# Optimization experiments

Hardware: AMD Instinct MI355X
Metric: run time of the kernel (lower is better)

Reference implementation:

```python
import jax, jax.numpy as jnp
import numpy as np

B, S, D, H, E, K = 4, 4096, 256, 1024, 8, 2


def setup_inputs() -> dict:
    key = jax.random.key(0)
    ks = jax.random.split(key, 7)
    sc = 0.02
    return {
        "x": jax.random.normal(ks[0], (B, S, D), dtype=jnp.float32),
        "w_router": jax.random.normal(ks[1], (D, E), dtype=jnp.float32) * sc,
        "b_router": jnp.zeros((E,), dtype=jnp.float32),
        "w1": jax.random.normal(ks[2], (E, D, H), dtype=jnp.float32) * sc,
        "b1": jnp.zeros((E, H), dtype=jnp.float32),
        "w2": jax.random.normal(ks[3], (E, H, D), dtype=jnp.float32) * sc,
        "b2": jnp.zeros((E, D), dtype=jnp.float32),
    }


def reference(x, w_router, b_router, w1, b1, w2, b2):
    # Router: softmax over experts, then top-k selection + renormalization
    router_logits = jnp.einsum("bsd,de->bse", x, w_router) + b_router
    router_probs = jax.nn.softmax(router_logits, axis=-1)            # [B,S,E]
    top_probs, top_idx = jax.lax.top_k(router_probs, K)               # [B,S,K]
    top_w = top_probs / jnp.sum(top_probs, axis=-1, keepdims=True)    # renorm

    # Combine weights per expert: sum_k one_hot(idx_k) * w_k  -> [B,S,E]
    combine = jnp.sum(jax.nn.one_hot(top_idx, E, dtype=x.dtype) * top_w[..., None], axis=-2)

    # Dense equivalent of the masked gather/scatter dispatch:
    # out[b,s] = sum_e combine[b,s,e] * Expert_e(x[b,s])
    h = jax.nn.gelu(jnp.einsum("bsd,edh->bseh", x, w1) + b1, approximate=False)  # [B,S,E,H]
    y = jnp.einsum("bseh,ehd->bsed", h, w2) + b2                                  # [B,S,E,D]
    out = jnp.einsum("bsed,bse->bsd", y, combine)                                  # [B,S,D]
    return out, router_probs
```

## Files before the change

### kernel.cpp

```cpp
#include <hip/hip_runtime.h>

typedef float f32x4 __attribute__((ext_vector_type(4)));
typedef short s16x8 __attribute__((ext_vector_type(8)));

static constexpr int NTOK = 16384;
static constexpr int D    = 256;
static constexpr int H    = 1024;
static constexpr int E    = 8;

__device__ __forceinline__ float bf2f(unsigned short u) {
    return __uint_as_float(((unsigned int)u) << 16);
}
__device__ __forceinline__ unsigned short f2bf(float f) {
    unsigned int u = __float_as_uint(f);
    u += 0x7FFFu + ((u >> 16) & 1u);
    return (unsigned short)(u >> 16);
}
__device__ __forceinline__ s16x8 pack8(float4 a, float4 b) {
    s16x8 v;
    v[0] = (short)f2bf(a.x); v[1] = (short)f2bf(a.y);
    v[2] = (short)f2bf(a.z); v[3] = (short)f2bf(a.w);
    v[4] = (short)f2bf(b.x); v[5] = (short)f2bf(b.y);
    v[6] = (short)f2bf(b.z); v[7] = (short)f2bf(b.w);
    return v;
}

__device__ __forceinline__ void barrier_lds_only() {
    __asm__ __volatile__("s_waitcnt lgkmcnt(0)" ::: "memory");
    __builtin_amdgcn_s_barrier();
    __asm__ __volatile__("" ::: "memory");
}

__global__ void __launch_bounds__(256) prep_kernel(
    const float* __restrict__ w1, const float* __restrict__ w2,
    unsigned short* __restrict__ w1t, unsigned short* __restrict__ w2t,
    const float* __restrict__ x, const float* __restrict__ wr,
    const float* __restrict__ br, float* __restrict__ probs_out,
    int* __restrict__ cnt, int* __restrict__ list, float* __restrict__ wlist)
{
    __shared__ __align__(16) char smem[9280];
    const int tid = threadIdx.x;

    if (blockIdx.x < 4096) {
        unsigned short (*tile)[33] = reinterpret_cast<unsigned short(*)[33]>(smem);
        int b = blockIdx.x;
        const float* src; unsigned short* dst;
        int Rr, Cc, tr, tc;
        if (b < 2048) {
            int e = b >> 8, tt = b & 255;
            Rr = 256; Cc = 1024; tr = tt >> 5; tc = tt & 31;
            src = w1 + (size_t)e * Rr * Cc; dst = w1t + (size_t)e * Rr * Cc;
        } else {
            b -= 2048;
            int e = b >> 8, tt = b & 255;
            Rr = 1024; Cc = 256; tr = tt >> 3; tc = tt & 7;
            src = w2 + (size_t)e * Rr * Cc; dst = w2t + (size_t)e * Rr * Cc;
        }
        const int c = tid & 31, r0 = tid >> 5;
        #pragma unroll
        for (int rr = 0; rr < 32; rr += 8)
            tile[r0 + rr][c] = f2bf(src[(size_t)(tr * 32 + r0 + rr) * Cc + tc * 32 + c]);
        __syncthreads();
        #pragma unroll
        for (int rr = 0; rr < 32; rr += 8)
            dst[(size_t)(tc * 32 + r0 + rr) * Rr + tr * 32 + c] = tile[c][r0 + rr];
    } else {
        float (*wrs)[9] = reinterpret_cast<float(*)[9]>(smem);
        int* lcnt  = reinterpret_cast<int*>(smem + 9216);
        int* gbase = lcnt + 8;

        if (tid < 8) lcnt[tid] = 0;
        {
            float4 a = *reinterpret_cast<const float4*>(wr + tid * 8);
            float4 b = *reinterpret_cast<const float4*>(wr + tid * 8 + 4);
            wrs[tid][0] = a.x; wrs[tid][1] = a.y; wrs[tid][2] = a.z; wrs[tid][3] = a.w;
            wrs[tid][4] = b.x; wrs[tid][5] = b.y; wrs[tid][6] = b.z; wrs[tid][7] = b.w;
        }
        __syncthreads();

        const int g = tid >> 4, l = tid & 15;
        const int t = (blockIdx.x - 4096) * 16 + g;

        float lg[8];
        #pragma unroll
        for (int e = 0; e < 8; ++e) lg[e] = 0.f;
        const float* xr = x + (size_t)t * D;
        #pragma unroll
        for (int r = 0; r < 4; ++r) {
            const int d = r * 64 + l * 4;
            float4 xv = *reinterpret_cast<const float4*>(xr + d);
            #pragma unroll
            for (int j = 0; j < 4; ++j) {
                const float xf = (j == 0) ? xv.x : (j == 1) ? xv.y : (j == 2) ? xv.z : xv.w;
                #pragma unroll
                for (int e = 0; e < 8; ++e) lg[e] += xf * wrs[d + j][e];
            }
        }
        #pragma unroll
        for (int off = 1; off < 16; off <<= 1)
            #pragma unroll
            for (int e = 0; e < 8; ++e) lg[e] += __shfl_xor(lg[e], off, 16);

        int i1 = 0, i2 = 0, lp1 = 0, lp2 = 0;
        float wa = 0.f, wb = 0.f;
        if (l == 0) {
            #pragma unroll
            for (int e = 0; e < 8; ++e) lg[e] += br[e];
            float mx = lg[0];
            #pragma unroll
            for (int e = 1; e < 8; ++e) mx = fmaxf(mx, lg[e]);
            float p[8], s = 0.f;
            #pragma unroll
            for (int e = 0; e < 8; ++e) { p[e] = expf(lg[e] - mx); s += p[e]; }
            const float inv = 1.f / s;
            #pragma unroll
            for (int e = 0; e < 8; ++e) p[e] *= inv;
            float4 o0 = {p[0], p[1], p[2], p[3]}, o1 = {p[4], p[5], p[6], p[7]};
            *reinterpret_cast<float4*>(probs_out + t * 8)     = o0;
            *reinterpret_cast<float4*>(probs_out + t * 8 + 4) = o1;

            #pragma unroll
            for (int e = 1; e < 8; ++e) if (p[e] > p[i1]) i1 = e;
            i2 = (i1 == 0) ? 1 : 0;
            #pragma unroll
            for (int e = 0; e < 8; ++e) if (e != i1 && p[e] > p[i2]) i2 = e;
            const float sw = p[i1] + p[i2];
            wa = p[i1] / sw; wb = p[i2] / sw;
            lp1 = atomicAdd(&lcnt[i1], 1);
            lp2 = atomicAdd(&lcnt[i2], 1);
        }
        __syncthreads();
        if (tid < 8) gbase[tid] = atomicAdd(&cnt[tid], lcnt[tid]);
        __syncthreads();
        if (l == 0) {
            int pos = gbase[i1] + lp1;
            list[i1 * NTOK + pos] = t;
            wlist[i1 * NTOK + pos] = wa;
            pos = gbase[i2] + lp2;
            list[i2 * NTOK + pos] = t | (1 << 30);
            wlist[i2 * NTOK + pos] = wb;
        }
    }
}

__global__ void __launch_bounds__(512, 4) expert_kernel_v6(
    const float* __restrict__ x,
    const unsigned short* __restrict__ w1t,
    const unsigned short* __restrict__ w2t,
    const float* __restrict__ b1,
    const float* __restrict__ b2,
    const int* __restrict__ cnt, const int* __restrict__ list,
    const float* __restrict__ wlist,
    float* __restrict__ out,
    float* __restrict__ ybuf32,
    unsigned short* __restrict__ ybuf16,
    const int mode)
{
    const int e = blockIdx.y;
    int n = cnt[e]; n = (n < 0) ? 0 : ((n > NTOK) ? NTOK : n);
    const int tile0 = blockIdx.x * 64;
    if (tile0 >= n) return;
    const int nvalid = (n - tile0 < 64) ? (n - tile0) : 64;

    __shared__ __align__(16) unsigned short W1s[2][32 * 264];
    __shared__ __align__(16) unsigned short W2s[2][256 * 32];
    __shared__ __align__(16) unsigned short Hs [2][64 * 40];
    __shared__ int   toks[64];
    __shared__ float wgts[64];

    const int tid  = threadIdx.x;
    const int lane = tid & 63;
    const int wv   = tid >> 6;
    const int mrow = lane & 15;
    const int kb   = lane >> 4;
    const int key4 = (mrow & 3) ^ ((mrow >> 2) & 3);
    const int rb    = wv & 3;
    const int chb   = wv >> 2;
    const int tpart = wv & 1;
    const int dpart = wv >> 1;

    if (tid < 64) {
        if (tid < nvalid) {
            toks[tid] = list[e * NTOK + tile0 + tid];
            wgts[tid] = wlist[e * NTOK + tile0 + tid];
        } else { toks[tid] = 0; wgts[tid] = 0.f; }
    }

    const size_t w1b = (size_t)e * H * D;
    const size_t w2b = (size_t)e * D * H;
    s16x8 pfW1[2], pfW2[2];

    #define LOADW1(HC)                                                                  \
        _Pragma("unroll")                                                               \
        for (int k = 0; k < 2; ++k) {                                                   \
            const int s = k * 512 + tid, h1 = s >> 5, c1 = s & 31;                      \
            pfW1[k] = *reinterpret_cast<const s16x8*>(                                  \
                w1t + w1b + (size_t)((HC) * 32 + h1) * D + c1 * 8);                     \
        }
    #define STOREW1(BUF)                                                                \
        _Pragma("unroll")                                                               \
        for (int k = 0; k < 2; ++k) {                                                   \
            const int s = k * 512 + tid, h1 = s >> 5, c1 = s & 31;                      \
            *reinterpret_cast<s16x8*>(&W1s[BUF][h1 * 264 + c1 * 8]) = pfW1[k];          \
        }
    #define LOADW2(HC)                                                                  \
        _Pragma("unroll")                                                               \
        for (int k = 0; k < 2; ++k) {                                                   \
            const int s = k * 512 + tid, d2 = s >> 2, c2 = s & 3;                       \
            pfW2[k] = *reinterpret_cast<const s16x8*>(                                  \
                w2t + w2b + (size_t)d2 * H + (HC) * 32 + c2 * 8);                       \
        }
    #define STOREW2(BUF)                                                                \
        _Pragma("unroll")                                                               \
        for (int k = 0; k < 2; ++k) {                                                   \
            const int s = k * 512 + tid, d2 = s >> 2, c2 = s & 3;                       \
            const int k2 = (d2 & 3) ^ ((d2 >> 2) & 3);                                  \
            *reinterpret_cast<s16x8*>(&W2s[BUF][d2 * 32 + ((c2 ^ k2) << 3)]) = pfW2[k]; \
        }

    LOADW1(0);
    __syncthreads();

    s16x8 aFrag[8];
    {
        const float* xrow = x + (size_t)(toks[rb * 16 + mrow] & 0x3FFF) * D;
        #pragma unroll
        for (int ks = 0; ks < 8; ++ks) {
            const float* src = xrow + ks * 32 + kb * 8;
            aFrag[ks] = pack8(*reinterpret_cast<const float4*>(src),
                              *reinterpret_cast<const float4*>(src + 4));
        }
    }

    STOREW1(0);
    LOADW1(1);
    LOADW2(0);
    __syncthreads();

    f32x4 accYt[2][4];
    #pragma unroll
    for (int i = 0; i < 2; ++i)
        #pragma unroll
        for (int j = 0; j < 4; ++j) accYt[i][j] = (f32x4){0.f, 0.f, 0.f, 0.f};

    for (int hc = 0; hc < 32; ++hc) {
        const int cur = hc & 1, nxt = cur ^ 1;

        if (hc < 31) { STOREW1(nxt); }
        if (hc < 30) { LOADW1(hc + 2); }
        STOREW2(cur);
        if (hc < 31) { LOADW2(hc + 1); }

        f32x4 accH = (f32x4){0.f, 0.f, 0.f, 0.f};
        {
            const int brow = chb * 16 + mrow;
            #pragma unroll
            for (int ks = 0; ks < 8; ++ks) {
                s16x8 bfrag = *reinterpret_cast<const s16x8*>(
                    &W1s[cur][brow * 264 + ks * 32 + kb * 8]);
                accH = __builtin_amdgcn_mfma_f32_16x16x32_bf16(aFrag[ks], bfrag, accH, 0, 0, 0);
            }
            const float bias = b1[e * H + hc * 32 + brow];
            #pragma unroll
            for (int r = 0; r < 4; ++r) {
                const int t = rb * 16 + kb * 4 + r;
                const float v = accH[r] + bias;
                const float u = v * (0.7978845608f + 0.0356774081f * v * v);
                const float g = __fdividef(v, 1.0f + __expf(-2.0f * u));
                Hs[cur][t * 40 + brow] = f2bf(g);
            }
        }

        if (hc > 0) {
            s16x8 bfrag[2];
            #pragma unroll
            for (int tg = 0; tg < 2; ++tg)
                bfrag[tg] = *reinterpret_cast<const s16x8*>(
                    &Hs[nxt][((tpart * 2 + tg) * 16 + mrow) * 40 + kb * 8]);
            #pragma unroll
            for (int db = 0; db < 4; ++db) {
                const int d = (dpart * 4 + db) * 16 + mrow;
                s16x8 afrag = *reinterpret_cast<const s16x8*>(
                    &W2s[nxt][d * 32 + ((kb ^ key4) << 3)]);
                #pragma unroll
                for (int tg = 0; tg < 2; ++tg)
                    accYt[tg][db] = __builtin_amdgcn_mfma_f32_16x16x32_bf16(
                        afrag, bfrag[tg], accYt[tg][db], 0, 0, 0);
            }
        }
        barrier_lds_only();
    }

    {
        s16x8 bfrag[2];
        #pragma unroll
        for (int tg = 0; tg < 2; ++tg)
            bfrag[tg] = *reinterpret_cast<const s16x8*>(
                &Hs[1][((tpart * 2 + tg) * 16 + mrow) * 40 + kb * 8]);
        #pragma unroll
        for (int db = 0; db < 4; ++db) {
            const int d = (dpart * 4 + db) * 16 + mrow;
            s16x8 afrag = *reinterpret_cast<const s16x8*>(
                &W2s[1][d * 32 + ((kb ^ key4) << 3)]);
            #pragma unroll
            for (int tg = 0; tg < 2; ++tg)
                accYt[tg][db] = __builtin_amdgcn_mfma_f32_16x16x32_bf16(
                    afrag, bfrag[tg], accYt[tg][db], 0, 0, 0);
        }
    }

    #pragma unroll
    for (int tg = 0; tg < 2; ++tg) {
        const int tloc = (tpart * 2 + tg) * 16 + mrow;
        if (tloc < nvalid) {
            const float wt = wgts[tloc];
            const int raw = toks[tloc];
            const int t = raw & 0x3FFF;
            const size_t slotbase = ((size_t)((raw >> 30) & 1) * NTOK + t) * D;
            if (mode == 1) {
                float* ybase = ybuf32 + slotbase;
                #pragma unroll
                for (int db = 0; db < 4; ++db) {
                    const int d0 = (dpart * 4 + db) * 16 + kb * 4;
                    const float4 bv = *reinterpret_cast<const float4*>(b2 + e * D + d0);
                    float4 v = {(accYt[tg][db][0] + bv.x) * wt, (accYt[tg][db][1] + bv.y) * wt,
                                (accYt[tg][db][2] + bv.z) * wt, (accYt[tg][db][3] + bv.w) * wt};
                    *reinterpret_cast<float4*>(ybase + d0) = v;
                }
            } else if (mode == 2) {
                unsigned short* ybase = ybuf16 + slotbase;
                #pragma unroll
                for (int db = 0; db < 4; ++db) {
                    const int d0 = (dpart * 4 + db) * 16 + kb * 4;
                    const float4 bv = *reinterpret_cast<const float4*>(b2 + e * D + d0);
                    ushort4 v;
                    v.x = f2bf((accYt[tg][db][0] + bv.x) * wt);
                    v.y = f2bf((accYt[tg][db][1] + bv.y) * wt);
                    v.z = f2bf((accYt[tg][db][2] + bv.z) * wt);
                    v.w = f2bf((accYt[tg][db][3] + bv.w) * wt);
                    *reinterpret_cast<ushort4*>(ybase + d0) = v;
                }
            } else {
                float* obase = out + (size_t)t * D;
                #pragma unroll
                for (int db = 0; db < 4; ++db) {
                    const int d0 = (dpart * 4 + db) * 16 + kb * 4;
                    const float4 bv = *reinterpret_cast<const float4*>(b2 + e * D + d0);
                    atomicAdd(obase + d0 + 0, (accYt[tg][db][0] + bv.x) * wt);
                    atomicAdd(obase + d0 + 1, (accYt[tg][db][1] + bv.y) * wt);
                    atomicAdd(obase + d0 + 2, (accYt[tg][db][2] + bv.z) * wt);
                    atomicAdd(obase + d0 + 3, (accYt[tg][db][3] + bv.w) * wt);
                }
            }
        }
    }
    #undef LOADW1
    #undef STOREW1
    #undef LOADW2
    #undef STOREW2
}

__global__ void __launch_bounds__(256) combine_f32_kernel(
    const float* __restrict__ ybuf, float* __restrict__ out)
{
    const size_t i = ((size_t)blockIdx.x * 256 + threadIdx.x) * 4;
    float4 a = *reinterpret_cast<const float4*>(ybuf + i);
    float4 b = *reinterpret_cast<const float4*>(ybuf + (size_t)NTOK * D + i);
    float4 v = {a.x + b.x, a.y + b.y, a.z + b.z, a.w + b.w};
    *reinterpret_cast<float4*>(out + i) = v;
}
__global__ void __launch_bounds__(256) combine_bf16_kernel(
    const unsigned short* __restrict__ ybuf, float* __restrict__ out)
{
    const size_t i = ((size_t)blockIdx.x * 256 + threadIdx.x) * 4;
    ushort4 a = *reinterpret_cast<const ushort4*>(ybuf + i);
    ushort4 b = *reinterpret_cast<const ushort4*>(ybuf + (size_t)NTOK * D + i);
    float4 v = {bf2f(a.x) + bf2f(b.x), bf2f(a.y) + bf2f(b.y),
                bf2f(a.z) + bf2f(b.z), bf2f(a.w) + bf2f(b.w)};
    *reinterpret_cast<float4*>(out + i) = v;
}

__global__ void __launch_bounds__(256) expert_kernel_fp32(
    const float* __restrict__ x, const float* __restrict__ w1, const float* __restrict__ w2,
    const float* __restrict__ b1, const float* __restrict__ b2,
    const int* __restrict__ cnt, const int* __restrict__ list, const float* __restrict__ wlist,
    float* __restrict__ out)
{
    const int e = blockIdx.y;
    int n = cnt[e]; n = (n < 0) ? 0 : ((n > NTOK) ? NTOK : n);
    const int tile0 = blockIdx.x * 64;
    if (tile0 >= n) return;
    const int nvalid = (n - tile0 < 64) ? (n - tile0) : 64;

    __shared__ __align__(16) unsigned short Xs [64 * 264];
    __shared__ __align__(16) unsigned short W1s[64 * 264];
    __shared__ __align__(16) unsigned short W2s[256 * 72];
    __shared__ __align__(16) unsigned short Hs [64 * 72];
    __shared__ int   toks[64];
    __shared__ float wgts[64];

    const int tid = threadIdx.x, lane = tid & 63, wv = tid >> 6;
    const int mrow = lane & 15, kb = lane >> 4;

    if (tid < 64) {
        if (tid < nvalid) {
            toks[tid] = list[e * NTOK + tile0 + tid] & 0x3FFF;
            wgts[tid] = wlist[e * NTOK + tile0 + tid];
        } else { toks[tid] = 0; wgts[tid] = 0.f; }
    }
    __syncthreads();

    #pragma unroll
    for (int r = 0; r < 8; ++r) {
        int v = r * 256 + tid, row = v >> 5, c8 = v & 31;
        s16x8 val = {0,0,0,0,0,0,0,0};
        if (row < nvalid) {
            const float* src = x + (size_t)toks[row] * D + c8 * 8;
            val = pack8(*reinterpret_cast<const float4*>(src),
                        *reinterpret_cast<const float4*>(src + 4));
        }
        *reinterpret_cast<s16x8*>(&Xs[row * 264 + c8 * 8]) = val;
    }

    f32x4 accYt[16];
    #pragma unroll
    for (int i = 0; i < 16; ++i) accYt[i] = (f32x4){0.f, 0.f, 0.f, 0.f};

    const int wr2 = wv >> 1, wc2 = wv & 1;
    const int hgrp = tid & 7, dblk = tid >> 3;
    const int dgrp = tid & 31, hblk8 = tid >> 5;

    for (int hc = 0; hc < 16; ++hc) {
        __syncthreads();
        {
            s16x8 Y8[8];
            #pragma unroll
            for (int i = 0; i < 8; ++i) {
                const float* src = w1 + ((size_t)(e * D + dblk * 8 + i)) * H + hc * 64 + hgrp * 8;
                Y8[i] = pack8(*reinterpret_cast<const float4*>(src),
                              *reinterpret_cast<const float4*>(src + 4));
            }
            #pragma unroll
            for (int j = 0; j < 8; ++j) {
                s16x8 V;
                #pragma unroll
                for (int i = 0; i < 8; ++i) V[i] = Y8[i][j];
                *reinterpret_cast<s16x8*>(&W1s[(hgrp * 8 + j) * 264 + dblk * 8]) = V;
            }
        }
        {
            s16x8 Z8[8];
            #pragma unroll
            for (int i = 0; i < 8; ++i) {
                const float* src = w2 + ((size_t)(e * H + hc * 64 + hblk8 * 8 + i)) * D + dgrp * 8;
                Z8[i] = pack8(*reinterpret_cast<const float4*>(src),
                              *reinterpret_cast<const float4*>(src + 4));
            }
            const int hswz = (hblk8 ^ (dgrp & 7)) << 3;
            #pragma unroll
            for (int j = 0; j < 8; ++j) {
                s16x8 V;
                #pragma unroll
                for (int i = 0; i < 8; ++i) V[i] = Z8[i][j];
                *reinterpret_cast<s16x8*>(&W2s[(dgrp * 8 + j) * 72 + hswz]) = V;
            }
        }
        __syncthreads();

        f32x4 accH[2][2];
        #pragma unroll
        for (int i = 0; i < 2; ++i)
            #pragma unroll
            for (int j = 0; j < 2; ++j) accH[i][j] = (f32x4){0.f, 0.f, 0.f, 0.f};
        #pragma unroll
        for (int ks = 0; ks < 8; ++ks) {
            const int koff = ks * 32 + kb * 8;
            s16x8 a0 = *reinterpret_cast<const s16x8*>(&Xs [((wr2*2+0)*16 + mrow)*264 + koff]);
            s16x8 a1 = *reinterpret_cast<const s16x8*>(&Xs [((wr2*2+1)*16 + mrow)*264 + koff]);
            s16x8 b0 = *reinterpret_cast<const s16x8*>(&W1s[((wc2*2+0)*16 + mrow)*264 + koff]);
            s16x8 b1v= *reinterpret_cast<const s16x8*>(&W1s[((wc2*2+1)*16 + mrow)*264 + koff]);
            accH[0][0] = __builtin_amdgcn_mfma_f32_16x16x32_bf16(a0, b0,  accH[0][0], 0, 0, 0);
            accH[0][1] = __builtin_amdgcn_mfma_f32_16x16x32_bf16(a0, b1v, accH[0][1], 0, 0, 0);
            accH[1][0] = __builtin_amdgcn_mfma_f32_16x16x32_bf16(a1, b0,  accH[1][0], 0, 0, 0);
            accH[1][1] = __builtin_amdgcn_mfma_f32_16x16x32_bf16(a1, b1v, accH[1][1], 0, 0, 0);
        }
        #pragma unroll
        for (int i = 0; i < 2; ++i)
            #pragma unroll
            for (int j = 0; j < 2; ++j) {
                const int hloc = (wc2*2 + j) * 16 + mrow;
                const float bias = b1[e * H + hc * 64 + hloc];
                #pragma unroll
                for (int r = 0; r < 4; ++r) {
                    const int m = (wr2*2 + i) * 16 + kb * 4 + r;
                    float vvf = accH[i][j][r] + bias;
                    float g = 0.5f * vvf * (1.0f + erff(vvf * 0.70710678118654752f));
                    Hs[m * 72 + hloc] = f2bf(g);
                }
            }
        __syncthreads();

        #pragma unroll
        for (int ks = 0; ks < 2; ++ks) {
            const int koff = ks * 32 + kb * 8;
            s16x8 bfrag = *reinterpret_cast<const s16x8*>(&Hs[(wv * 16 + mrow) * 72 + koff]);
            #pragma unroll
            for (int db = 0; db < 16; ++db) {
                const int arow = db * 16 + mrow;
                const int akey = (arow >> 3) & 7;
                s16x8 afrag = *reinterpret_cast<const s16x8*>(
                    &W2s[arow * 72 + (((ks * 4 + kb) ^ akey) << 3)]);
                accYt[db] = __builtin_amdgcn_mfma_f32_16x16x32_bf16(afrag, bfrag, accYt[db], 0, 0, 0);
            }
        }
    }

    {
        const int t = wv * 16 + mrow;
        if (t < nvalid) {
            const float wt = wgts[t];
            float* obase = out + (size_t)toks[t] * D;
            #pragma unroll
            for (int db = 0; db < 16; ++db) {
                const int d0 = db * 16 + kb * 4;
                #pragma unroll
                for (int r = 0; r < 4; ++r)
                    atomicAdd(obase + d0 + r, (accYt[db][r] + b2[e * D + d0 + r]) * wt);
            }
        }
    }
}

extern "C" void kernel_launch(void* const* d_in, const int* in_sizes, int n_in,
                              void* d_out, int out_size, void* d_ws, size_t ws_size,
                              hipStream_t stream)
{
    const float* x  = (const float*)d_in[0];
    const float* wr = (const float*)d_in[1];
    const float* br = (const float*)d_in[2];
    const float* w1 = (const float*)d_in[3];
    const float* b1 = (const float*)d_in[4];
    const float* w2 = (const float*)d_in[5];
    const float* b2 = (const float*)d_in[6];
    float* out = (float*)d_out;

    char* ws = (char*)d_ws;
    int*   cnt   = (int*)ws;
    int*   list  = (int*)(ws + 256);
    float* wlist = (float*)(ws + 524544);
    unsigned short* w1t = (unsigned short*)(ws + 1048832);
    unsigned short* w2t = (unsigned short*)(ws + 5243136);
    float*          ybuf32 = (float*)(ws + 9437440);
    unsigned short* ybuf16 = (unsigned short*)(ws + 9437440);

    const bool big = ws_size >= 9437440;
    int mode = 0;
    if (big) {
        if (ws_size >= 9437440ull + 33554432ull)      mode = 1;
        else if (ws_size >= 9437440ull + 16777216ull) mode = 2;
    }

    if (mode == 0)
        hipMemsetAsync(out, 0, (size_t)NTOK * D * 4, stream);
    hipMemsetAsync(cnt, 0, 256, stream);
    if (big) {
        prep_kernel<<<5120, 256, 0, stream>>>(w1, w2, w1t, w2t,
                                              x, wr, br, out + (size_t)NTOK * D, cnt, list, wlist);
        expert_kernel_v6<<<dim3(256, 8), 512, 0, stream>>>(
            x, w1t, w2t, b1, b2, cnt, list, wlist, out, ybuf32, ybuf16, mode);
        if (mode == 1)
            combine_f32_kernel<<<(NTOK * D / 4) / 256, 256, 0, stream>>>(ybuf32, out);
        else if (mode == 2)
            combine_bf16_kernel<<<(NTOK * D / 4) / 256, 256, 0, stream>>>(ybuf16, out);
    } else {
        prep_kernel<<<5120, 256, 0, stream>>>(w1, w2, w1t, w2t,
                                              x, wr, br, out + (size_t)NTOK * D, cnt, list, wlist);
        expert_kernel_fp32<<<dim3(256, 8), 256, 0, stream>>>(x, w1, w2, b1, b2, cnt, list, wlist, out);
    }
}
```

Before: 226.1 us.

## Load W1 MFMA fragments directly from global memory into registers, dropping LDS staging

Removes the shared-memory double buffer for W1. Each wave now prefetches its W1 B-fragments straight from global memory into registers, one chunk ahead, and feeds them to the MFMAs. This cuts LDS traffic and LDS footprint and removes the W1 store step in the loop. In exchange, each W1 chunk is loaded redundantly by the waves that share it (different rb) through L2/L1, and register pressure rises with eight extra prefetch fragments under the 512x4 launch bound.

```diff
diff --git a/kernel.cpp b/kernel.cpp
--- a/kernel.cpp
+++ b/kernel.cpp
@@ -143,7 +143,7 @@
     }
 }
 
-__global__ void __launch_bounds__(512, 4) expert_kernel_v6(
+__global__ void __launch_bounds__(512, 4) expert_kernel_v7(
     const float* __restrict__ x,
     const unsigned short* __restrict__ w1t,
     const unsigned short* __restrict__ w2t,
@@ -162,7 +162,6 @@
     if (tile0 >= n) return;
     const int nvalid = (n - tile0 < 64) ? (n - tile0) : 64;
 
-    __shared__ __align__(16) unsigned short W1s[2][32 * 264];
     __shared__ __align__(16) unsigned short W2s[2][256 * 32];
     __shared__ __align__(16) unsigned short Hs [2][64 * 40];
     __shared__ int   toks[64];
@@ -185,24 +184,29 @@
             wgts[tid] = wlist[e * NTOK + tile0 + tid];
         } else { toks[tid] = 0; wgts[tid] = 0.f; }
     }
-
-    const size_t w1b = (size_t)e * H * D;
+    __syncthreads();
+
+    s16x8 aFrag[8];
+    {
+        const float* xrow = x + (size_t)(toks[rb * 16 + mrow] & 0x3FFF) * D;
+        #pragma unroll
+        for (int ks = 0; ks < 8; ++ks) {
+            const float* src = xrow + ks * 32 + kb * 8;
+            aFrag[ks] = pack8(*reinterpret_cast<const float4*>(src),
+                              *reinterpret_cast<const float4*>(src + 4));
+        }
+    }
+
     const size_t w2b = (size_t)e * D * H;
-    s16x8 pfW1[2], pfW2[2];
-
-    #define LOADW1(HC)                                                                  \
+    const unsigned short* w1row = w1t + (size_t)e * H * D + (size_t)(chb * 16 + mrow) * D + kb * 8;
+    s16x8 pfB1[8];
+    s16x8 pfW2[2];
+
+    #define LOADB1(HC)                                                                  \
         _Pragma("unroll")                                                               \
-        for (int k = 0; k < 2; ++k) {                                                   \
-            const int s = k * 512 + tid, h1 = s >> 5, c1 = s & 31;                      \
-            pfW1[k] = *reinterpret_cast<const s16x8*>(                                  \
-                w1t + w1b + (size_t)((HC) * 32 + h1) * D + c1 * 8);                     \
-        }
-    #define STOREW1(BUF)                                                                \
-        _Pragma("unroll")                                                               \
-        for (int k = 0; k < 2; ++k) {                                                   \
-            const int s = k * 512 + tid, h1 = s >> 5, c1 = s & 31;                      \
-            *reinterpret_cast<s16x8*>(&W1s[BUF][h1 * 264 + c1 * 8]) = pfW1[k];          \
-        }
+        for (int ks = 0; ks < 8; ++ks)                                                  \
+            pfB1[ks] = *reinterpret_cast<const s16x8*>(                                 \
+                w1row + (size_t)(HC) * 32 * D + ks * 32);
     #define LOADW2(HC)                                                                  \
         _Pragma("unroll")                                                               \
         for (int k = 0; k < 2; ++k) {                                                   \
@@ -218,24 +222,8 @@
             *reinterpret_cast<s16x8*>(&W2s[BUF][d2 * 32 + ((c2 ^ k2) << 3)]) = pfW2[k]; \
         }
 
-    LOADW1(0);
-    __syncthreads();
-
-    s16x8 aFrag[8];
-    {
-        const float* xrow = x + (size_t)(toks[rb * 16 + mrow] & 0x3FFF) * D;
-        #pragma unroll
-        for (int ks = 0; ks < 8; ++ks) {
-            const float* src = xrow + ks * 32 + kb * 8;
-            aFrag[ks] = pack8(*reinterpret_cast<const float4*>(src),
-                              *reinterpret_cast<const float4*>(src + 4));
-        }
-    }
-
-    STOREW1(0);
-    LOADW1(1);
+    LOADB1(0);
     LOADW2(0);
-    __syncthreads();
 
     f32x4 accYt[2][4];
     #pragma unroll
@@ -246,20 +234,17 @@
     for (int hc = 0; hc < 32; ++hc) {
         const int cur = hc & 1, nxt = cur ^ 1;
 
-        if (hc < 31) { STOREW1(nxt); }
-        if (hc < 30) { LOADW1(hc + 2); }
         STOREW2(cur);
         if (hc < 31) { LOADW2(hc + 1); }
 
         f32x4 accH = (f32x4){0.f, 0.f, 0.f, 0.f};
         {
+            #pragma unroll
+            for (int ks = 0; ks < 8; ++ks)
+                accH = __builtin_amdgcn_mfma_f32_16x16x32_bf16(aFrag[ks], pfB1[ks], accH, 0, 0, 0);
+            if (hc < 31) { LOADB1(hc + 1); }
+
             const int brow = chb * 16 + mrow;
-            #pragma unroll
-            for (int ks = 0; ks < 8; ++ks) {
-                s16x8 bfrag = *reinterpret_cast<const s16x8*>(
-                    &W1s[cur][brow * 264 + ks * 32 + kb * 8]);
-                accH = __builtin_amdgcn_mfma_f32_16x16x32_bf16(aFrag[ks], bfrag, accH, 0, 0, 0);
-            }
             const float bias = b1[e * H + hc * 32 + brow];
             #pragma unroll
             for (int r = 0; r < 4; ++r) {
@@ -354,8 +339,7 @@
             }
         }
     }
-    #undef LOADW1
-    #undef STOREW1
+    #undef LOADB1
     #undef LOADW2
     #undef STOREW2
 }
@@ -566,7 +550,7 @@
     if (big) {
         prep_kernel<<<5120, 256, 0, stream>>>(w1, w2, w1t, w2t,
                                               x, wr, br, out + (size_t)NTOK * D, cnt, list, wlist);
-        expert_kernel_v6<<<dim3(256, 8), 512, 0, stream>>>(
+        expert_kernel_v7<<<dim3(256, 8), 512, 0, stream>>>(
             x, w1t, w2t, b1, b2, cnt, list, wlist, out, ybuf32, ybuf16, mode);
         if (mode == 1)
             combine_f32_kernel<<<(NTOK * D / 4) / 256, 256, 0, stream>>>(ybuf32, out);
```

After: 359.6 us. +59.1%, slower.
